# Optimization experiments

Measured on AMD Instinct MI355X. Metric: run time of the kernel, lower is better.

The kernel has to match this reference:

```python
import jax, jax.numpy as jnp
import numpy as np

HEADS = 16

def setup_inputs() -> dict:
    key = jax.random.key(0)
    k1, k2, k3 = jax.random.split(key, 3)
    T, B, E = 2048, 4, 1024
    query = jax.random.normal(k1, (T, B, E), dtype=jnp.float32)
    in_proj_weight = jax.random.normal(k2, (3 * E, E), dtype=jnp.float32) * (E ** -0.5)
    out_proj_weight = jax.random.normal(k3, (E, E), dtype=jnp.float32) * (E ** -0.5)
    return {"query": query, "in_proj_weight": in_proj_weight, "out_proj_weight": out_proj_weight}

def reference(query, in_proj_weight, out_proj_weight):
    # query: [T, B, E] (time-first, as in apex SelfMultiheadAttn)
    T, B, E = query.shape
    H = HEADS
    D = E // H
    scale = D ** -0.5
    # fused in-projection: x @ W_in^T -> [T, B, 3E]
    qkv = jnp.einsum('tbe,fe->tbf', query, in_proj_weight)
    q, k, v = jnp.split(qkv, 3, axis=-1)
    # [T, B, E] -> [B, H, T, D]
    def to_bhtd(x):
        return x.reshape(T, B, H, D).transpose(1, 2, 0, 3)
    q = to_bhtd(q) * scale
    k = to_bhtd(k)
    v = to_bhtd(v)
    scores = jnp.einsum('bhqd,bhkd->bhqk', q, k)  # [B, H, T, T]
    # causal (mask_future_timesteps=True) time mask
    causal = jnp.tril(jnp.ones((T, T), dtype=bool))
    scores = jnp.where(causal, scores, jnp.finfo(scores.dtype).min)
    attn = jax.nn.softmax(scores, axis=-1)
    # dropout_prob = 0.0 -> identity
    ctx = jnp.einsum('bhqk,bhkd->bhqd', attn, v)  # [B, H, T, D]
    ctx = ctx.transpose(2, 0, 1, 3).reshape(T, B, E)
    out = jnp.einsum('tbe,fe->tbf', ctx, out_proj_weight)
    return out
```

## Files before the change

kernel.cpp:

```cpp
#include <hip/hip_runtime.h>


typedef float  f32x4  __attribute__((ext_vector_type(4)));
typedef short  s16x8  __attribute__((ext_vector_type(8)));
typedef __bf16 bf16x8 __attribute__((ext_vector_type(8)));

#define T_DIM 2048
#define B_DIM 4
#define E_DIM 1024
#define PLANE (T_DIM * 64)

__device__ inline unsigned short f2bf(float f) {
  return (unsigned short)((__builtin_bit_cast(unsigned int, f) + 0x8000u) >> 16);
}

__device__ inline f32x4 mfma16(s16x8 a, s16x8 b, f32x4 c) {
  return __builtin_amdgcn_mfma_f32_16x16x32_bf16(
      __builtin_bit_cast(bf16x8, a), __builtin_bit_cast(bf16x8, b), c, 0, 0, 0);
}

__device__ inline void gl2lds16(const unsigned short* g, unsigned short* l) {
  __builtin_amdgcn_global_load_lds(
      (__attribute__((address_space(1))) unsigned int*)g,
      (__attribute__((address_space(3))) unsigned int*)l, 16, 0, 0);
}

__device__ inline unsigned packbf(float a, float b) {
  return __builtin_amdgcn_perm(__builtin_bit_cast(unsigned, b),
                               __builtin_bit_cast(unsigned, a), 0x07060302u);
}

__global__ __launch_bounds__(256)
void cvt_all(const float* __restrict__ q, const float* __restrict__ wi,
             const float* __restrict__ wo, unsigned short* __restrict__ xb,
             unsigned short* __restrict__ wib, unsigned short* __restrict__ wob,
             float qs, int do_wout) {
  int blk = blockIdx.x;
  const float* src;
  unsigned short* dst;
  int i;
  float sc = 1.0f;
  if (blk < 8192) {
    src = q; dst = xb; i = blk * 256 + threadIdx.x;
  } else if (blk < 11264) {
    src = wi; dst = wib; i = (blk - 8192) * 256 + threadIdx.x;
    if (i < (E_DIM * E_DIM / 4)) sc = qs;
  } else {
    if (!do_wout) return;
    src = wo; dst = wob; i = (blk - 11264) * 256 + threadIdx.x;
  }
  float4 v = ((const float4*)src)[i];
  ushort4 o;
  o.x = f2bf(v.x * sc); o.y = f2bf(v.y * sc);
  o.z = f2bf(v.z * sc); o.w = f2bf(v.w * sc);
  ((ushort4*)dst)[i] = o;
}

__global__ __launch_bounds__(256)
void cvt_bf16(const float* __restrict__ in, unsigned short* __restrict__ out,
              int n4) {
  int i = blockIdx.x * 256 + threadIdx.x;
  if (i >= n4) return;
  float4 v = ((const float4*)in)[i];
  ushort4 o;
  o.x = f2bf(v.x); o.y = f2bf(v.y); o.z = f2bf(v.z); o.w = f2bf(v.w);
  ((ushort4*)out)[i] = o;
}

__global__ __launch_bounds__(256, 2)
void gemm256(const unsigned short* __restrict__ A,
             const unsigned short* __restrict__ Bw,
             unsigned short* __restrict__ Cq, int K) {
  __shared__ __attribute__((aligned(16))) unsigned short As[256 * 64];
  __shared__ __attribute__((aligned(16))) unsigned short Bs[128 * 64];

  const int tid = threadIdx.x, lane = tid & 63, w = tid >> 6;
  const int row16 = lane & 15, quad = lane >> 4;
  const int m0 = blockIdx.y * 256, n0 = blockIdx.x * 128;
  const int wm = (w & 1) * 128, wn = (w >> 1) * 64;
  const int srow = lane >> 3;
  const int jsw = (lane & 7) ^ srow;
  const int sw7 = row16 & 7;

  f32x4 acc[8][4];
  for (int i = 0; i < 8; ++i)
    for (int j = 0; j < 4; ++j) acc[i][j] = (f32x4){0.f, 0.f, 0.f, 0.f};

  for (int k0 = 0; k0 < K; k0 += 64) {
    for (int i2 = 0; i2 < 8; ++i2) {
      int ia = w * 8 + i2;
      int r = ia * 8 + srow;
      gl2lds16(A + (size_t)(m0 + r) * K + k0 + jsw * 8, &As[ia * 512]);
    }
    for (int i2 = 0; i2 < 4; ++i2) {
      int ib = w * 4 + i2;
      int r = ib * 8 + srow;
      gl2lds16(Bw + (size_t)(n0 + r) * K + k0 + jsw * 8, &Bs[ib * 512]);
    }
    __syncthreads();
    for (int kk = 0; kk < 2; ++kk) {
      s16x8 af[8], bfr[4];
      for (int mi = 0; mi < 8; ++mi)
        af[mi] = *(const s16x8*)&As[(wm + mi * 16 + row16) * 64 +
                                    (((kk * 4 + quad) ^ sw7) * 8)];
      for (int ni = 0; ni < 4; ++ni)
        bfr[ni] = *(const s16x8*)&Bs[(wn + ni * 16 + row16) * 64 +
                                     (((kk * 4 + quad) ^ sw7) * 8)];
      for (int mi = 0; mi < 8; ++mi)
        for (int ni = 0; ni < 4; ++ni)
          acc[mi][ni] = mfma16(af[mi], bfr[ni], acc[mi][ni]);
    }
    __syncthreads();
  }

  if (n0 >= 2048) {
    const int hw = ((n0 & 1023) >> 6) + (w >> 1);
    const int tg0 = (m0 >> 2) + (w & 1) * 32;
    unsigned short* tb = &As[w * 2560];
    for (int bb = 0; bb < 4; ++bb) {
      for (int mi = 0; mi < 8; ++mi)
        for (int ni = 0; ni < 4; ++ni)
          tb[(ni * 16 + row16) * 40 + mi * 4 + quad] = f2bf(acc[mi][ni][bb]);
      asm volatile("s_waitcnt lgkmcnt(0)" ::: "memory");
      unsigned short* vp = Cq + (size_t)(128 + bb * 16 + hw) * PLANE;
      for (int it = 0; it < 4; ++it) {
        int dd = it * 16 + (lane >> 2);
        int tl = (lane & 3) * 8;
        s16x8 v = *(const s16x8*)&tb[dd * 40 + tl];
        *(s16x8*)(vp + (size_t)dd * T_DIM + tg0 + tl) = v;
      }
      asm volatile("s_waitcnt lgkmcnt(0)" ::: "memory");
    }
  } else {
    for (int mi = 0; mi < 8; ++mi)
      for (int ni = 0; ni < 4; ++ni)
        for (int r = 0; r < 4; ++r) {
          int m = m0 + wm + mi * 16 + quad * 4 + r;
          int n = n0 + wn + ni * 16 + row16;
          int t = m >> 2, bb = m & 3;
          int which = n >> 10, hh = (n >> 6) & 15, dd = n & 63;
          Cq[(size_t)(which * 64 + bb * 16 + hh) * PLANE + (size_t)t * 64 + dd] =
              f2bf(acc[mi][ni][r]);
        }
  }
}

__global__ __launch_bounds__(256)
void gemm128(const unsigned short* __restrict__ A,
             const unsigned short* __restrict__ Bw,
             float* __restrict__ Cf, int N, int K) {
  __shared__ __attribute__((aligned(16))) unsigned short As[128 * 64];
  __shared__ __attribute__((aligned(16))) unsigned short Bs[128 * 64];

  const int tid = threadIdx.x, lane = tid & 63, w = tid >> 6;
  const int row16 = lane & 15, quad = lane >> 4;
  const int m0 = blockIdx.y * 128, n0 = blockIdx.x * 128;
  const int wm = (w & 1) * 64, wn = (w >> 1) * 64;
  const int srow = lane >> 3;
  const int jsw = (lane & 7) ^ srow;
  const int sw7 = row16 & 7;

  f32x4 acc[4][4];
  for (int i = 0; i < 4; ++i)
    for (int j = 0; j < 4; ++j) acc[i][j] = (f32x4){0.f, 0.f, 0.f, 0.f};

  for (int k0 = 0; k0 < K; k0 += 64) {
    for (int i = 0; i < 4; ++i) {
      int ia = i * 4 + w;
      int r = ia * 8 + srow;
      gl2lds16(A  + (size_t)(m0 + r) * K + k0 + jsw * 8, &As[ia * 512]);
      gl2lds16(Bw + (size_t)(n0 + r) * K + k0 + jsw * 8, &Bs[ia * 512]);
    }
    __syncthreads();
    for (int kk = 0; kk < 2; ++kk) {
      s16x8 af[4], bfr[4];
      for (int mi = 0; mi < 4; ++mi)
        af[mi] = *(const s16x8*)&As[(wm + mi * 16 + row16) * 64 +
                                    (((kk * 4 + quad) ^ sw7) * 8)];
      for (int ni = 0; ni < 4; ++ni)
        bfr[ni] = *(const s16x8*)&Bs[(wn + ni * 16 + row16) * 64 +
                                     (((kk * 4 + quad) ^ sw7) * 8)];
      for (int mi = 0; mi < 4; ++mi)
        for (int ni = 0; ni < 4; ++ni)
          acc[mi][ni] = mfma16(af[mi], bfr[ni], acc[mi][ni]);
    }
    __syncthreads();
  }

  for (int mi = 0; mi < 4; ++mi)
    for (int ni = 0; ni < 4; ++ni)
      for (int r = 0; r < 4; ++r) {
        int m = m0 + wm + mi * 16 + quad * 4 + r;
        int n = n0 + wn + ni * 16 + row16;
        Cf[(size_t)m * N + n] = acc[mi][ni][r];
      }
}

__global__ __launch_bounds__(512, 4)
void attn_fwd(const unsigned short* __restrict__ qkv,
              unsigned short* __restrict__ ctx) {
  __shared__ __attribute__((aligned(16))) unsigned short Ks[2][4096];
  __shared__ __attribute__((aligned(16))) unsigned short Vs[2][4096];
  __shared__ __attribute__((aligned(16))) unsigned short Ps[8][1024];

  const int tid = threadIdx.x, lane = tid & 63, w = tid >> 6;
  const int row16 = lane & 15, quad = lane >> 4;
  const int bh = blockIdx.x;
  const int p  = blockIdx.y;
  const int b = bh >> 4, h = bh & 15;

  const unsigned short* Qg = qkv + (size_t)bh * PLANE;
  const unsigned short* Kg = qkv + (size_t)(64 + bh) * PLANE;
  const unsigned short* Vt = qkv + (size_t)(128 + bh) * PLANE;

  const int r8 = lane >> 3;
  const int jsw = (lane & 7) ^ r8;
  const int sw7 = row16 & 7;

  auto stage = [&](int c, int buf) {
    int r = w * 8 + r8;
    gl2lds16(Kg + (size_t)(c * 64 + r) * 64 + jsw * 8, &Ks[buf][w * 512]);
    gl2lds16(Vt + (size_t)r * T_DIM + c * 64 + jsw * 8, &Vs[buf][w * 512]);
  };

  for (int half = 0; half < 2; ++half) {
    const int qt = half ? p : (15 - p);
    const int q0w = qt * 128 + w * 16;
    const int cmax = 2 * qt + 1;
    const int dc = 2 * qt + (w >> 2);

    s16x8 qb[2];
    for (int s = 0; s < 2; ++s)
      qb[s] = *(const s16x8*)(Qg + (size_t)(q0w + row16) * 64 + s * 32 +
                              quad * 8);

    f32x4 O[4];
    for (int md = 0; md < 4; ++md) O[md] = (f32x4){0.f, 0.f, 0.f, 0.f};
    float lp = 0.f;

    stage(0, 0);
    stage(1, 1);

    for (int c = 0; c <= cmax; ++c) {
      const int buf = c & 1;
      if (c < cmax) asm volatile("s_waitcnt vmcnt(2)" ::: "memory");
      else          asm volatile("s_waitcnt vmcnt(0)" ::: "memory");
      __builtin_amdgcn_s_barrier();

      if (c <= dc) {
        f32x4 S[4];
        for (int nt = 0; nt < 4; ++nt) S[nt] = (f32x4){0.f, 0.f, 0.f, 0.f};
        __builtin_amdgcn_s_setprio(1);
        for (int nt = 0; nt < 4; ++nt)
          for (int s = 0; s < 2; ++s) {
            s16x8 ka = *(const s16x8*)&Ks[buf][(nt * 16 + row16) * 64 +
                                              (((s * 4 + quad) ^ sw7) * 8)];
            S[nt] = mfma16(ka, qb[s], S[nt]);
          }
        __builtin_amdgcn_s_setprio(0);

        const int qg = q0w + row16;
        auto softmax_store = [&](bool diagm) {
          for (int nt = 0; nt < 4; ++nt) {
            float pv[4];
            for (int r = 0; r < 4; ++r) {
              pv[r] = __builtin_amdgcn_exp2f(S[nt][r]);
              if (diagm && (c * 64 + nt * 16 + quad * 4 + r) > qg) pv[r] = 0.f;
              lp += pv[r];
            }
            int pos = (nt * 2 + (quad >> 1)) ^ sw7;
            *(uint2*)&Ps[w][row16 * 64 + pos * 8 + (quad & 1) * 4] =
                make_uint2(packbf(pv[0], pv[1]), packbf(pv[2], pv[3]));
          }
        };
        if (c == dc) softmax_store(true); else softmax_store(false);
        asm volatile("s_waitcnt lgkmcnt(0)" ::: "memory");

        __builtin_amdgcn_s_setprio(1);
        for (int sk = 0; sk < 2; ++sk) {
          s16x8 pb = *(const s16x8*)&Ps[w][row16 * 64 +
                                          (((sk * 4 + quad) ^ sw7) * 8)];
          for (int md = 0; md < 4; ++md) {
            s16x8 va = *(const s16x8*)&Vs[buf][(md * 16 + row16) * 64 +
                                              (((sk * 4 + quad) ^ sw7) * 8)];
            O[md] = mfma16(va, pb, O[md]);
          }
        }
        __builtin_amdgcn_s_setprio(0);
      }

      __builtin_amdgcn_s_barrier();
      if (c + 2 <= cmax) stage(c + 2, buf);
    }

    {
      float s = lp;
      s += __shfl_xor(s, 16);
      s += __shfl_xor(s, 32);
      float inv = 1.f / s;
      const int t = q0w + row16;
      for (int md = 0; md < 4; ++md) {
        unsigned lo = packbf(O[md][0] * inv, O[md][1] * inv);
        unsigned hi = packbf(O[md][2] * inv, O[md][3] * inv);
        *(uint2*)&ctx[((size_t)t * B_DIM + b) * E_DIM + h * 64 + md * 16 +
                      quad * 4] = make_uint2(lo, hi);
      }
    }
  }
}

extern "C" void kernel_launch(void* const* d_in, const int* in_sizes, int n_in,
                              void* d_out, int out_size, void* d_ws,
                              size_t ws_size, hipStream_t stream) {
  const float* query = (const float*)d_in[0];
  const float* win   = (const float*)d_in[1];
  const float* wout  = (const float*)d_in[2];
  float* out = (float*)d_out;

  const size_t qkv_el = (size_t)3 * 64 * PLANE;
  const size_t ctx_el = (size_t)T_DIM * B_DIM * E_DIM;

  unsigned short* qkvb = (unsigned short*)d_ws;
  unsigned short* ctxb = qkvb + qkv_el;
  unsigned short* xb   = ctxb;
  unsigned short* winb = (unsigned short*)d_out;

  const bool big_ws = ws_size >= (qkv_el + ctx_el + (size_t)E_DIM * E_DIM) * 2;
  unsigned short* woutb = big_ws ? (ctxb + ctx_el) : qkvb;

  const float QSCALE = 0.18033688011112042f;

  cvt_all<<<big_ws ? 12288 : 11264, 256, 0, stream>>>(
      query, win, wout, xb, winb, woutb, QSCALE, big_ws ? 1 : 0);
  gemm256<<<dim3(3072 / 128, 8192 / 256), 256, 0, stream>>>(xb, winb, qkvb,
                                                            1024);
  attn_fwd<<<dim3(64, 8), 512, 0, stream>>>(qkvb, ctxb);
  if (!big_ws)
    cvt_bf16<<<1024, 256, 0, stream>>>(wout, woutb, (1024 * 1024) / 4);
  gemm128<<<dim3(8, 64), 256, 0, stream>>>(ctxb, woutb, out, 1024, 1024);
}
```

Before: 223.8 us.

## Rework QKV GEMM into 256x256 tiles with 8 waves and double-buffered pipelined staging

The in-projection GEMM grows from a 256x128 tile with 4 waves to a 256x256 tile with 8 waves. It double-buffers A and B in LDS, split into halves, and interleaves the async global-to-LDS loads for upcoming k-tiles with MFMA quarters, using fine-grained vmcnt waits and barriers. The aim is to hide global load latency behind compute and raise arithmetic intensity per block. In exchange it uses more LDS (128KB) and adds many barriers, which may limit occupancy. The epilogue index mapping is adjusted to match the new wave-to-tile layout.

```diff
diff --git a/kernel.cpp b/kernel.cpp
--- a/kernel.cpp
+++ b/kernel.cpp
@@ -9,6 +9,10 @@
 #define B_DIM 4
 #define E_DIM 1024
 #define PLANE (T_DIM * 64)
+
+#define VMC(N) asm volatile("s_waitcnt vmcnt(" #N ")" ::: "memory")
+#define LGKM0() asm volatile("s_waitcnt lgkmcnt(0)" ::: "memory")
+#define BAR() __builtin_amdgcn_s_barrier()
 
 __device__ inline unsigned short f2bf(float f) {
   return (unsigned short)((__builtin_bit_cast(unsigned int, f) + 0x8000u) >> 16);
@@ -67,76 +71,135 @@
   ((ushort4*)out)[i] = o;
 }
 
-__global__ __launch_bounds__(256, 2)
+__global__ __launch_bounds__(512, 2)
 void gemm256(const unsigned short* __restrict__ A,
              const unsigned short* __restrict__ Bw,
              unsigned short* __restrict__ Cq, int K) {
-  __shared__ __attribute__((aligned(16))) unsigned short As[256 * 64];
-  __shared__ __attribute__((aligned(16))) unsigned short Bs[128 * 64];
+  __shared__ __attribute__((aligned(16))) unsigned short As[2][2][8192];
+  __shared__ __attribute__((aligned(16))) unsigned short Bs[2][2][8192];
 
   const int tid = threadIdx.x, lane = tid & 63, w = tid >> 6;
   const int row16 = lane & 15, quad = lane >> 4;
-  const int m0 = blockIdx.y * 256, n0 = blockIdx.x * 128;
-  const int wm = (w & 1) * 128, wn = (w >> 1) * 64;
-  const int srow = lane >> 3;
-  const int jsw = (lane & 7) ^ srow;
+  const int m0 = blockIdx.y * 256, n0 = blockIdx.x * 256;
+  const int r8 = lane >> 3;
+  const int jsw = (lane & 7) ^ r8;
   const int sw7 = row16 & 7;
 
   f32x4 acc[8][4];
+#pragma unroll
   for (int i = 0; i < 8; ++i)
+#pragma unroll
     for (int j = 0; j < 4; ++j) acc[i][j] = (f32x4){0.f, 0.f, 0.f, 0.f};
 
-  for (int k0 = 0; k0 < K; k0 += 64) {
-    for (int i2 = 0; i2 < 8; ++i2) {
-      int ia = w * 8 + i2;
-      int r = ia * 8 + srow;
-      gl2lds16(A + (size_t)(m0 + r) * K + k0 + jsw * 8, &As[ia * 512]);
-    }
-    for (int i2 = 0; i2 < 4; ++i2) {
-      int ib = w * 4 + i2;
-      int r = ib * 8 + srow;
-      gl2lds16(Bw + (size_t)(n0 + r) * K + k0 + jsw * 8, &Bs[ib * 512]);
-    }
-    __syncthreads();
-    for (int kk = 0; kk < 2; ++kk) {
-      s16x8 af[8], bfr[4];
-      for (int mi = 0; mi < 8; ++mi)
-        af[mi] = *(const s16x8*)&As[(wm + mi * 16 + row16) * 64 +
-                                    (((kk * 4 + quad) ^ sw7) * 8)];
-      for (int ni = 0; ni < 4; ++ni)
-        bfr[ni] = *(const s16x8*)&Bs[(wn + ni * 16 + row16) * 64 +
-                                     (((kk * 4 + quad) ^ sw7) * 8)];
-      for (int mi = 0; mi < 8; ++mi)
-        for (int ni = 0; ni < 4; ++ni)
-          acc[mi][ni] = mfma16(af[mi], bfr[ni], acc[mi][ni]);
-    }
-    __syncthreads();
+  auto stageA = [&](int tile, int half) {
+#pragma unroll
+    for (int i2 = 0; i2 < 2; ++i2) {
+      int ia = w * 2 + i2;
+      gl2lds16(A + (size_t)(m0 + half * 128 + ia * 8 + r8) * K + tile * 64 +
+                   jsw * 8,
+               &As[tile & 1][half][ia * 512]);
+    }
+  };
+  auto stageB = [&](int tile, int half) {
+#pragma unroll
+    for (int i2 = 0; i2 < 2; ++i2) {
+      int ia = w * 2 + i2;
+      gl2lds16(Bw + (size_t)(n0 + half * 128 + ia * 8 + r8) * K + tile * 64 +
+                    jsw * 8,
+               &Bs[tile & 1][half][ia * 512]);
+    }
+  };
+
+  s16x8 a[4][2], bq[4][2];
+
+  auto lda = [&](int buf, int mlo) {
+#pragma unroll
+    for (int mi2 = 0; mi2 < 4; ++mi2)
+#pragma unroll
+      for (int s = 0; s < 2; ++s)
+        a[mi2][s] = *(const s16x8*)&As[buf][mlo >> 2]
+            [((w & 1) * 64 + mi2 * 16 + row16) * 64 +
+             (((s * 4 + quad) ^ sw7) * 8)];
+  };
+  auto ldb = [&](int buf) {
+#pragma unroll
+    for (int ni = 0; ni < 4; ++ni)
+#pragma unroll
+      for (int s = 0; s < 2; ++s)
+        bq[ni][s] = *(const s16x8*)&Bs[buf][w >> 2]
+            [(((w >> 1) & 1) * 64 + ni * 16 + row16) * 64 +
+             (((s * 4 + quad) ^ sw7) * 8)];
+  };
+  auto mm = [&](int mlo, int nlo) {
+    __builtin_amdgcn_s_setprio(1);
+#pragma unroll
+    for (int mi2 = 0; mi2 < 4; ++mi2)
+#pragma unroll
+      for (int ni2 = 0; ni2 < 2; ++ni2)
+#pragma unroll
+        for (int s = 0; s < 2; ++s)
+          acc[mlo + mi2][nlo + ni2] =
+              mfma16(a[mi2][s], bq[nlo + ni2][s], acc[mlo + mi2][nlo + ni2]);
+    __builtin_amdgcn_s_setprio(0);
+  };
+
+  const int NJ = K / 128;
+
+  stageA(0, 0); stageA(0, 1); stageB(0, 0); stageB(0, 1); stageA(1, 0);
+
+  for (int j = 0; j < NJ; ++j) {
+    const int t = 2 * j;
+    const bool full = (j < NJ - 1);
+    stageA(t + 1, 1);
+    VMC(4);
+    BAR(); lda(0, 0); ldb(0); mm(0, 0); LGKM0(); BAR();
+    stageB(t + 1, 0);
+    BAR(); mm(0, 2); LGKM0(); BAR();
+    stageB(t + 1, 1);
+    VMC(12);
+    BAR(); lda(0, 4); mm(4, 0); LGKM0(); BAR();
+    if (full) stageA(t + 2, 0);
+    BAR(); mm(4, 2); LGKM0(); BAR();
+    if (full) { stageA(t + 2, 1); VMC(4); } else { VMC(0); }
+    BAR(); lda(1, 0); ldb(1); mm(0, 0); LGKM0(); BAR();
+    if (full) stageB(t + 2, 0);
+    BAR(); mm(0, 2); LGKM0(); BAR();
+    if (full) { stageB(t + 2, 1); VMC(12); } else { VMC(4); }
+    BAR(); lda(1, 4); mm(4, 0); LGKM0(); BAR();
+    if (full) stageA(t + 3, 0);
+    BAR(); mm(4, 2); LGKM0(); BAR();
   }
 
   if (n0 >= 2048) {
     const int hw = ((n0 & 1023) >> 6) + (w >> 1);
-    const int tg0 = (m0 >> 2) + (w & 1) * 32;
-    unsigned short* tb = &As[w * 2560];
+    unsigned short* tb = &As[0][0][0] + w * 2560;
     for (int bb = 0; bb < 4; ++bb) {
+#pragma unroll
       for (int mi = 0; mi < 8; ++mi)
-        for (int ni = 0; ni < 4; ++ni)
-          tb[(ni * 16 + row16) * 40 + mi * 4 + quad] = f2bf(acc[mi][ni][bb]);
-      asm volatile("s_waitcnt lgkmcnt(0)" ::: "memory");
+#pragma unroll
+        for (int ni = 0; ni < 4; ++ni) {
+          int tloc = (mi & 3) * 4 + quad + (mi >> 2) * 16;
+          tb[(ni * 16 + row16) * 40 + tloc] = f2bf(acc[mi][ni][bb]);
+        }
+      LGKM0();
       unsigned short* vp = Cq + (size_t)(128 + bb * 16 + hw) * PLANE;
+#pragma unroll
       for (int it = 0; it < 4; ++it) {
         int dd = it * 16 + (lane >> 2);
         int tl = (lane & 3) * 8;
         s16x8 v = *(const s16x8*)&tb[dd * 40 + tl];
-        *(s16x8*)(vp + (size_t)dd * T_DIM + tg0 + tl) = v;
+        int tg = (m0 >> 2) + (w & 1) * 16 + (tl >> 4) * 32 + (tl & 15);
+        *(s16x8*)(vp + (size_t)dd * T_DIM + tg) = v;
       }
-      asm volatile("s_waitcnt lgkmcnt(0)" ::: "memory");
+      LGKM0();
     }
   } else {
     for (int mi = 0; mi < 8; ++mi)
       for (int ni = 0; ni < 4; ++ni)
         for (int r = 0; r < 4; ++r) {
-          int m = m0 + wm + mi * 16 + quad * 4 + r;
-          int n = n0 + wn + ni * 16 + row16;
+          int m = m0 + (w & 1) * 64 + (mi >> 2) * 128 + (mi & 3) * 16 +
+                  quad * 4 + r;
+          int n = n0 + (w >> 1) * 64 + ni * 16 + row16;
           int t = m >> 2, bb = m & 3;
           int which = n >> 10, hh = (n >> 6) & 15, dd = n & 63;
           Cq[(size_t)(which * 64 + bb * 16 + hh) * PLANE + (size_t)t * 64 + dd] =
@@ -243,9 +306,9 @@
 
     for (int c = 0; c <= cmax; ++c) {
       const int buf = c & 1;
-      if (c < cmax) asm volatile("s_waitcnt vmcnt(2)" ::: "memory");
-      else          asm volatile("s_waitcnt vmcnt(0)" ::: "memory");
-      __builtin_amdgcn_s_barrier();
+      if (c < cmax) VMC(2);
+      else          VMC(0);
+      BAR();
 
       if (c <= dc) {
         f32x4 S[4];
@@ -274,7 +337,7 @@
           }
         };
         if (c == dc) softmax_store(true); else softmax_store(false);
-        asm volatile("s_waitcnt lgkmcnt(0)" ::: "memory");
+        LGKM0();
 
         __builtin_amdgcn_s_setprio(1);
         for (int sk = 0; sk < 2; ++sk) {
@@ -289,7 +352,7 @@
         __builtin_amdgcn_s_setprio(0);
       }
 
-      __builtin_amdgcn_s_barrier();
+      BAR();
       if (c + 2 <= cmax) stage(c + 2, buf);
     }
 
@@ -332,7 +395,7 @@
 
   cvt_all<<<big_ws ? 12288 : 11264, 256, 0, stream>>>(
       query, win, wout, xb, winb, woutb, QSCALE, big_ws ? 1 : 0);
-  gemm256<<<dim3(3072 / 128, 8192 / 256), 256, 0, stream>>>(xb, winb, qkvb,
+  gemm256<<<dim3(3072 / 256, 8192 / 256), 512, 0, stream>>>(xb, winb, qkvb,
                                                             1024);
   attn_fwd<<<dim3(64, 8), 512, 0, stream>>>(qkvb, ctxb);
   if (!big_ws)
```

Result: slower. 235.2 us (+5.1%).
